# Kernel tuning notes

Hardware: AMD Instinct MI355X
Metric: run time of the kernel (lower is better)

The kernel has to match this reference:

```python
import jax, jax.numpy as jnp
import numpy as np

MAX_LAG_FRACTION = 0.25
EPS = 1e-8
B, T = 1024, 2048


def setup_inputs() -> dict:
    key = jax.random.key(0)
    k1, k2, k3 = jax.random.split(key, 3)
    alpha_pred = jax.random.uniform(k1, (B,), dtype=jnp.float32)          # alpha in [0,1)
    D0_pred = jax.random.uniform(k2, (B,), dtype=jnp.float32)             # D0 in [0,1)
    trajectory = jax.random.normal(k3, (B, T, 2), dtype=jnp.float32)
    return {"alpha_pred": alpha_pred, "D0_pred": D0_pred, "trajectory": trajectory}


def _msd_all_lags(traj, max_lag):
    # traj: (B, T, C). Returns empirical MSD per sample per lag: (B, max_lag).
    Bn, Tn, _ = traj.shape
    t = jnp.arange(Tn)

    def step(carry, lag):
        idx = jnp.clip(t + lag, 0, Tn - 1)                    # (T,)
        disp = jnp.take(traj, idx, axis=1) - traj             # (B, T, C)
        sq = jnp.sum(disp * disp, axis=-1)                    # (B, T) squared displacement
        valid = (t + lag < Tn).astype(sq.dtype)               # (T,) mask for t in [0, T-lag)
        msd = jnp.sum(sq * valid[None, :], axis=-1) / jnp.maximum(jnp.sum(valid), 1.0)
        return carry, msd                                      # (B,)

    lags = jnp.arange(1, max_lag + 1)
    _, msd = jax.lax.scan(step, None, lags)                   # (max_lag, B)
    return msd.T                                               # (B, max_lag)


def reference(alpha_pred, D0_pred, trajectory):
    Bn, Tn, _ = trajectory.shape
    max_lag = max(1, int(Tn * MAX_LAG_FRACTION))
    msd_emp = _msd_all_lags(trajectory, max_lag)                               # (B, L)
    lags = jnp.arange(1, max_lag + 1, dtype=trajectory.dtype)                  # (L,)
    msd_theo = 4.0 * D0_pred[:, None] * jnp.power(lags[None, :], alpha_pred[:, None])  # (B, L)
    d = jnp.log(msd_theo + EPS) - jnp.log(msd_emp + EPS)
    # per-sample MSE over lags, then mean over batch (same as original loop)
    return jnp.mean(jnp.mean(d * d, axis=-1))
```

## Files before the change

### kernel.cpp

```cpp
#include <hip/hip_runtime.h>

#define B_SAMPLES 1024
#define T_LEN     2048
#define NLAG      512
#define ROWW      172

typedef __fp16   half2_t __attribute__((ext_vector_type(2)));
typedef _Float16 half8_t __attribute__((ext_vector_type(8)));
typedef float    floatx4 __attribute__((ext_vector_type(4)));

__device__ __forceinline__ int slotP(int k) { return k + (k >> 5); }

__global__ __launch_bounds__(256) void msd_mfma_kernel(
    const float* __restrict__ alpha, const float* __restrict__ d0p,
    const float* __restrict__ traj, float* __restrict__ partial) {
  const int b   = blockIdx.x;
  const int tid = threadIdx.x;
  const int w   = tid >> 6;
  const int l   = tid & 63;
  const int g   = l >> 4;
  const int p16 = l & 15;

  __shared__ __align__(16) unsigned int Zw[16 * ROWW];
  __shared__ float Pb[2116];
  __shared__ float Elds[33][16];
  __shared__ float cT[4];
  __shared__ float wred[4];

  for (int k = tid; k < 16 * 44; k += 256)
    Zw[(k / 44) * ROWW + 128 + (k % 44)] = 0u;

  const float4* tr4 = reinterpret_cast<const float4*>(traj) + (size_t)b * (T_LEN / 2);
  float sq[8];
  #pragma unroll
  for (int s = 0; s < 4; ++s) {
    int idx = (w << 8) + (l << 2) + s;
    float4 v4 = tr4[idx];
    int t0 = idx << 1;
    _Float16 hx0 = (_Float16)v4.x, hy0 = (_Float16)v4.y;
    _Float16 hx1 = (_Float16)v4.z, hy1 = (_Float16)v4.w;
    unsigned int wd0 = (unsigned int)__builtin_bit_cast(unsigned short, hx0)
                     | ((unsigned int)__builtin_bit_cast(unsigned short, hy0) << 16);
    unsigned int wd1 = (unsigned int)__builtin_bit_cast(unsigned short, hx1)
                     | ((unsigned int)__builtin_bit_cast(unsigned short, hy1) << 16);
    Zw[(t0 & 15) * ROWW + (t0 >> 4)] = wd0;
    Zw[((t0 + 1) & 15) * ROWW + ((t0 + 1) >> 4)] = wd1;
    float fx0 = (float)hx0, fy0 = (float)hy0;
    float fx1 = (float)hx1, fy1 = (float)hy1;
    sq[2 * s]     = fmaf(fx0, fx0, fy0 * fy0);
    sq[2 * s + 1] = fmaf(fx1, fx1, fy1 * fy1);
  }

  float ls = ((sq[0] + sq[1]) + (sq[2] + sq[3])) + ((sq[4] + sq[5]) + (sq[6] + sq[7]));
  float run = ls;
  #pragma unroll
  for (int dlt = 1; dlt < 64; dlt <<= 1) {
    float tsh = __shfl_up(run, dlt, 64);
    if (l >= dlt) run += tsh;
  }
  float excl = run - ls;
  if (l == 63) cT[w] = run;

  __syncthreads();

  float c0 = cT[0], c1 = cT[1], c2 = cT[2], c3 = cT[3];
  const float Ptot = (c0 + c1) + (c2 + c3);
  float off = 0.f;
  if (w > 0) off += c0;
  if (w > 1) off += c1;
  if (w > 2) off += c2;
  float r2 = off + excl;
  if (w == 0 || w == 3) {
    #pragma unroll
    for (int i = 0; i < 8; ++i) {
      r2 += sq[i];
      Pb[slotP((w << 9) + (l << 3) + i + 1)] = r2;
    }
  } else if (w == 2 && l == 63) {
    float r3 = r2 + ((sq[0] + sq[1]) + (sq[2] + sq[3])) +
               ((sq[4] + sq[5]) + (sq[6] + sq[7]));
    Pb[slotP(1536)] = r3;
  }

  const unsigned int* zrow = &Zw[p16 * ROWW];
  const int vS = 8 * w;

  floatx4 D[9];
  #pragma unroll
  for (int r = 0; r < 9; ++r) D[r] = (floatx4){0.f, 0.f, 0.f, 0.f};

  #pragma unroll
  for (int q = 0; q < 8; ++q) {
    const unsigned int* wp = zrow + 16 * q + 4 * g + vS;
    uint4 w0 = *reinterpret_cast<const uint4*>(wp);
    uint4 w1 = *reinterpret_cast<const uint4*>(wp + 4);
    uint4 w2 = *reinterpret_cast<const uint4*>(wp + 8);
    unsigned int win[12] = {w0.x, w0.y, w0.z, w0.w,  w1.x, w1.y, w1.z, w1.w,
                            w2.x, w2.y, w2.z, w2.w};
    uint4 aw = *reinterpret_cast<const uint4*>(zrow + 16 * q + 4 * g);
    half8_t aq = __builtin_bit_cast(half8_t, aw);
    #pragma unroll
    for (int r = 0; r < 9; ++r) {
      uint4 bw;
      bw.x = win[r]; bw.y = win[r + 1]; bw.z = win[r + 2]; bw.w = win[r + 3];
      half8_t bf = __builtin_bit_cast(half8_t, bw);
      D[r] = __builtin_amdgcn_mfma_f32_16x16x32_f16(aq, bf, D[r], 0, 0, 0);
    }
  }

  float accA[9], accB[9];
  #pragma unroll
  for (int r = 0; r < 9; ++r) { accA[r] = 0.f; accB[r] = 0.f; }

  const int rotb = 4 * g + p16;
  const int idx0 = (l & 48) << 2;

  #pragma unroll
  for (int rr = 0; rr < 4; ++rr) {
    const int src  = idx0 | (((rotb + rr) & 15) << 2);
    const bool wrap = (rotb + rr) >= 16;
    #pragma unroll
    for (int pr = 0; pr < 4; ++pr) {
      half2_t pk = __builtin_amdgcn_cvt_pkrtz(D[2 * pr][rr], D[2 * pr + 1][rr]);
      int got = __builtin_amdgcn_ds_bpermute(src, __builtin_bit_cast(int, pk));
      half2_t gh = __builtin_bit_cast(half2_t, got);
      float lo = (float)gh[0], hi = (float)gh[1];
      accA[2 * pr]     += wrap ? 0.f : lo;
      accB[2 * pr]     += wrap ? lo : 0.f;
      accA[2 * pr + 1] += wrap ? 0.f : hi;
      accB[2 * pr + 1] += wrap ? hi : 0.f;
    }
    {
      int got = __builtin_amdgcn_ds_bpermute(src, __builtin_bit_cast(int, D[8][rr]));
      float gv = __builtin_bit_cast(float, got);
      accA[8] += wrap ? 0.f : gv;
      accB[8] += wrap ? gv : 0.f;
    }
  }

  #pragma unroll
  for (int k = 0; k < 4; ++k) {
    float e0 = accA[2 * k]     + accB[2 * k + 1];
    float e1 = accA[2 * k + 1] + accB[2 * k + 2];
    half2_t pk = __builtin_amdgcn_cvt_pkrtz(e0, e1);
    half2_t t1 = __builtin_bit_cast(half2_t,
        __shfl_xor(__builtin_bit_cast(int, pk), 16, 64));
    pk = pk + t1;
    half2_t t2 = __builtin_bit_cast(half2_t,
        __shfl_xor(__builtin_bit_cast(int, pk), 32, 64));
    pk = pk + t2;
    if (l < 16) {
      Elds[vS + 2 * k][p16]     = (float)pk[0];
      Elds[vS + 2 * k + 1][p16] = (float)pk[1];
    }
  }
  if (w == 3) {
    float E = accA[8];
    E += __shfl_xor(E, 16, 64);
    E += __shfl_xor(E, 32, 64);
    if (l == 0) Elds[32][0] = E;
  }
  __syncthreads();

  const float aexp = alpha[b];
  const float c4d0 = 4.f * d0p[b];
  float loc = 0.f;
  #pragma unroll
  for (int c = 0; c < 2; ++c) {
    int lag = c * 256 + tid + 1;
    float E  = Elds[lag >> 4][lag & 15];
    float Pl = Pb[slotP(lag)];
    int mm   = 2048 - lag;
    float Pr = Pb[slotP(mm)];
    float S2  = Pr + (Ptot - Pl);
    float msd = fmaxf((S2 - 2.f * E) / (float)mm, 0.f);
    float theo = c4d0 * __builtin_exp2f(aexp * __builtin_log2f((float)lag));
    float dd = 0.69314718f * (__builtin_log2f(theo + 1e-8f) - __builtin_log2f(msd + 1e-8f));
    loc = fmaf(dd, dd, loc);
  }

  #pragma unroll
  for (int dlt = 1; dlt < 64; dlt <<= 1) loc += __shfl_xor(loc, dlt, 64);
  if (l == 0) wred[w] = loc;
  __syncthreads();
  if (tid == 0) partial[b] = (wred[0] + wred[1]) + (wred[2] + wred[3]);
}

__global__ __launch_bounds__(256) void reduce_kernel(
    const float* __restrict__ partial, float* __restrict__ out) {
  __shared__ float wsum[4];
  float acc = 0.f;
  for (int i = threadIdx.x; i < B_SAMPLES; i += 256) acc += partial[i];
  for (int off = 32; off > 0; off >>= 1) acc += __shfl_down(acc, off, 64);
  const int wid  = threadIdx.x >> 6;
  const int lane = threadIdx.x & 63;
  if (lane == 0) wsum[wid] = acc;
  __syncthreads();
  if (threadIdx.x == 0) {
    float t = wsum[0] + wsum[1] + wsum[2] + wsum[3];
    out[0] = t * (1.0f / ((float)B_SAMPLES * (float)NLAG));
  }
}

extern "C" void kernel_launch(void* const* d_in, const int* in_sizes, int n_in,
                              void* d_out, int out_size, void* d_ws, size_t ws_size,
                              hipStream_t stream) {
  const float* alpha = (const float*)d_in[0];
  const float* d0p   = (const float*)d_in[1];
  const float* traj  = (const float*)d_in[2];
  float* out     = (float*)d_out;
  float* partial = (float*)d_ws;

  msd_mfma_kernel<<<B_SAMPLES, 256, 0, stream>>>(alpha, d0p, traj, partial);
  reduce_kernel<<<1, 256, 0, stream>>>(partial, out);
}
```

Measured before the change: 16.31 us.

## Split each sample's MFMA lag work across eight waves instead of four

The per-sample block grows from 256 to 512 threads, so each wave handles four lag-row tiles (5 accumulators) instead of eight (9 accumulators). The prefix-sum, partial stores, bpermute reduction and final log loss are all re-indexed for 8 waves, with one lag per thread. The aim is shorter per-wave dependency chains, lower register pressure and more latency hiding per CU. The cost is more redundant A-fragment loads and a larger cross-wave scan and reduction per block.

After: 15.92 us. 2.4% less time.

```diff
diff --git a/kernel.cpp b/kernel.cpp
--- a/kernel.cpp
+++ b/kernel.cpp
@@ -11,7 +11,7 @@
 
 __device__ __forceinline__ int slotP(int k) { return k + (k >> 5); }
 
-__global__ __launch_bounds__(256) void msd_mfma_kernel(
+__global__ __launch_bounds__(512, 8) void msd_mfma_kernel(
     const float* __restrict__ alpha, const float* __restrict__ d0p,
     const float* __restrict__ traj, float* __restrict__ partial) {
   const int b   = blockIdx.x;
@@ -24,17 +24,17 @@
   __shared__ __align__(16) unsigned int Zw[16 * ROWW];
   __shared__ float Pb[2116];
   __shared__ float Elds[33][16];
-  __shared__ float cT[4];
-  __shared__ float wred[4];
-
-  for (int k = tid; k < 16 * 44; k += 256)
+  __shared__ float cT[8];
+  __shared__ float wred[8];
+
+  for (int k = tid; k < 16 * 44; k += 512)
     Zw[(k / 44) * ROWW + 128 + (k % 44)] = 0u;
 
   const float4* tr4 = reinterpret_cast<const float4*>(traj) + (size_t)b * (T_LEN / 2);
-  float sq[8];
-  #pragma unroll
-  for (int s = 0; s < 4; ++s) {
-    int idx = (w << 8) + (l << 2) + s;
+  float sq[4];
+  #pragma unroll
+  for (int s = 0; s < 2; ++s) {
+    int idx = (w << 7) + (l << 1) + s;
     float4 v4 = tr4[idx];
     int t0 = idx << 1;
     _Float16 hx0 = (_Float16)v4.x, hy0 = (_Float16)v4.y;
@@ -51,7 +51,7 @@
     sq[2 * s + 1] = fmaf(fx1, fx1, fy1 * fy1);
   }
 
-  float ls = ((sq[0] + sq[1]) + (sq[2] + sq[3])) + ((sq[4] + sq[5]) + (sq[6] + sq[7]));
+  float ls = (sq[0] + sq[1]) + (sq[2] + sq[3]);
   float run = ls;
   #pragma unroll
   for (int dlt = 1; dlt < 64; dlt <<= 1) {
@@ -64,53 +64,62 @@
   __syncthreads();
 
   float c0 = cT[0], c1 = cT[1], c2 = cT[2], c3 = cT[3];
-  const float Ptot = (c0 + c1) + (c2 + c3);
+  float c4 = cT[4], c5 = cT[5], c6 = cT[6], c7 = cT[7];
+  const float Ptot = ((c0 + c1) + (c2 + c3)) + ((c4 + c5) + (c6 + c7));
   float off = 0.f;
   if (w > 0) off += c0;
   if (w > 1) off += c1;
   if (w > 2) off += c2;
+  if (w > 3) off += c3;
+  if (w > 4) off += c4;
+  if (w > 5) off += c5;
+  if (w > 6) off += c6;
   float r2 = off + excl;
-  if (w == 0 || w == 3) {
+  if (w < 2 || w > 4) {
     #pragma unroll
-    for (int i = 0; i < 8; ++i) {
+    for (int i = 0; i < 4; ++i) {
       r2 += sq[i];
-      Pb[slotP((w << 9) + (l << 3) + i + 1)] = r2;
-    }
-  } else if (w == 2 && l == 63) {
-    float r3 = r2 + ((sq[0] + sq[1]) + (sq[2] + sq[3])) +
-               ((sq[4] + sq[5]) + (sq[6] + sq[7]));
-    Pb[slotP(1536)] = r3;
+      Pb[slotP((w << 8) + (l << 2) + i + 1)] = r2;
+    }
   }
 
   const unsigned int* zrow = &Zw[p16 * ROWW];
-  const int vS = 8 * w;
-
-  floatx4 D[9];
-  #pragma unroll
-  for (int r = 0; r < 9; ++r) D[r] = (floatx4){0.f, 0.f, 0.f, 0.f};
+  const int vS = 4 * w;
+
+  floatx4 D[5];
+  #pragma unroll
+  for (int r = 0; r < 5; ++r) D[r] = (floatx4){0.f, 0.f, 0.f, 0.f};
 
   #pragma unroll
   for (int q = 0; q < 8; ++q) {
     const unsigned int* wp = zrow + 16 * q + 4 * g + vS;
     uint4 w0 = *reinterpret_cast<const uint4*>(wp);
     uint4 w1 = *reinterpret_cast<const uint4*>(wp + 4);
-    uint4 w2 = *reinterpret_cast<const uint4*>(wp + 8);
-    unsigned int win[12] = {w0.x, w0.y, w0.z, w0.w,  w1.x, w1.y, w1.z, w1.w,
-                            w2.x, w2.y, w2.z, w2.w};
     uint4 aw = *reinterpret_cast<const uint4*>(zrow + 16 * q + 4 * g);
     half8_t aq = __builtin_bit_cast(half8_t, aw);
-    #pragma unroll
-    for (int r = 0; r < 9; ++r) {
-      uint4 bw;
-      bw.x = win[r]; bw.y = win[r + 1]; bw.z = win[r + 2]; bw.w = win[r + 3];
-      half8_t bf = __builtin_bit_cast(half8_t, bw);
-      D[r] = __builtin_amdgcn_mfma_f32_16x16x32_f16(aq, bf, D[r], 0, 0, 0);
-    }
-  }
-
-  float accA[9], accB[9];
-  #pragma unroll
-  for (int r = 0; r < 9; ++r) { accA[r] = 0.f; accB[r] = 0.f; }
+    {
+      D[0] = __builtin_amdgcn_mfma_f32_16x16x32_f16(aq, __builtin_bit_cast(half8_t, w0), D[0], 0, 0, 0);
+    }
+    {
+      uint4 bw; bw.x = w0.y; bw.y = w0.z; bw.z = w0.w; bw.w = w1.x;
+      D[1] = __builtin_amdgcn_mfma_f32_16x16x32_f16(aq, __builtin_bit_cast(half8_t, bw), D[1], 0, 0, 0);
+    }
+    {
+      uint4 bw; bw.x = w0.z; bw.y = w0.w; bw.z = w1.x; bw.w = w1.y;
+      D[2] = __builtin_amdgcn_mfma_f32_16x16x32_f16(aq, __builtin_bit_cast(half8_t, bw), D[2], 0, 0, 0);
+    }
+    {
+      uint4 bw; bw.x = w0.w; bw.y = w1.x; bw.z = w1.y; bw.w = w1.z;
+      D[3] = __builtin_amdgcn_mfma_f32_16x16x32_f16(aq, __builtin_bit_cast(half8_t, bw), D[3], 0, 0, 0);
+    }
+    {
+      D[4] = __builtin_amdgcn_mfma_f32_16x16x32_f16(aq, __builtin_bit_cast(half8_t, w1), D[4], 0, 0, 0);
+    }
+  }
+
+  float accA[5], accB[5];
+  #pragma unroll
+  for (int r = 0; r < 5; ++r) { accA[r] = 0.f; accB[r] = 0.f; }
 
   const int rotb = 4 * g + p16;
   const int idx0 = (l & 48) << 2;
@@ -120,7 +129,7 @@
     const int src  = idx0 | (((rotb + rr) & 15) << 2);
     const bool wrap = (rotb + rr) >= 16;
     #pragma unroll
-    for (int pr = 0; pr < 4; ++pr) {
+    for (int pr = 0; pr < 2; ++pr) {
       half2_t pk = __builtin_amdgcn_cvt_pkrtz(D[2 * pr][rr], D[2 * pr + 1][rr]);
       int got = __builtin_amdgcn_ds_bpermute(src, __builtin_bit_cast(int, pk));
       half2_t gh = __builtin_bit_cast(half2_t, got);
@@ -131,15 +140,15 @@
       accB[2 * pr + 1] += wrap ? hi : 0.f;
     }
     {
-      int got = __builtin_amdgcn_ds_bpermute(src, __builtin_bit_cast(int, D[8][rr]));
+      int got = __builtin_amdgcn_ds_bpermute(src, __builtin_bit_cast(int, D[4][rr]));
       float gv = __builtin_bit_cast(float, got);
-      accA[8] += wrap ? 0.f : gv;
-      accB[8] += wrap ? gv : 0.f;
-    }
-  }
-
-  #pragma unroll
-  for (int k = 0; k < 4; ++k) {
+      accA[4] += wrap ? 0.f : gv;
+      accB[4] += wrap ? gv : 0.f;
+    }
+  }
+
+  #pragma unroll
+  for (int k = 0; k < 2; ++k) {
     float e0 = accA[2 * k]     + accB[2 * k + 1];
     float e1 = accA[2 * k + 1] + accB[2 * k + 2];
     half2_t pk = __builtin_amdgcn_cvt_pkrtz(e0, e1);
@@ -154,8 +163,8 @@
       Elds[vS + 2 * k + 1][p16] = (float)pk[1];
     }
   }
-  if (w == 3) {
-    float E = accA[8];
+  if (w == 7) {
+    float E = accA[4];
     E += __shfl_xor(E, 16, 64);
     E += __shfl_xor(E, 32, 64);
     if (l == 0) Elds[32][0] = E;
@@ -164,10 +173,9 @@
 
   const float aexp = alpha[b];
   const float c4d0 = 4.f * d0p[b];
-  float loc = 0.f;
-  #pragma unroll
-  for (int c = 0; c < 2; ++c) {
-    int lag = c * 256 + tid + 1;
+  float loc;
+  {
+    int lag = tid + 1;
     float E  = Elds[lag >> 4][lag & 15];
     float Pl = Pb[slotP(lag)];
     int mm   = 2048 - lag;
@@ -176,14 +184,17 @@
     float msd = fmaxf((S2 - 2.f * E) / (float)mm, 0.f);
     float theo = c4d0 * __builtin_exp2f(aexp * __builtin_log2f((float)lag));
     float dd = 0.69314718f * (__builtin_log2f(theo + 1e-8f) - __builtin_log2f(msd + 1e-8f));
-    loc = fmaf(dd, dd, loc);
+    loc = dd * dd;
   }
 
   #pragma unroll
   for (int dlt = 1; dlt < 64; dlt <<= 1) loc += __shfl_xor(loc, dlt, 64);
   if (l == 0) wred[w] = loc;
   __syncthreads();
-  if (tid == 0) partial[b] = (wred[0] + wred[1]) + (wred[2] + wred[3]);
+  if (tid == 0) {
+    partial[b] = ((wred[0] + wred[1]) + (wred[2] + wred[3])) +
+                 ((wred[4] + wred[5]) + (wred[6] + wred[7]));
+  }
 }
 
 __global__ __launch_bounds__(256) void reduce_kernel(
@@ -211,6 +222,6 @@
   float* out     = (float*)d_out;
   float* partial = (float*)d_ws;
 
-  msd_mfma_kernel<<<B_SAMPLES, 256, 0, stream>>>(alpha, d0p, traj, partial);
+  msd_mfma_kernel<<<B_SAMPLES, 512, 0, stream>>>(alpha, d0p, traj, partial);
   reduce_kernel<<<1, 256, 0, stream>>>(partial, out);
 }
```
